# Kernel optimization log

Measured on AMD Instinct MI355X. Metric: run time of the kernel, lower is better.

The kernel has to match this reference:

```python
import jax, jax.numpy as jnp
import numpy as np

B, C, T = 256, 1, 16384   # batch, input_channels, seq_len
H = C                      # hidden_size == input_channels in this module
OUT = 1                    # output_channels


def setup_inputs() -> dict:
    key = jax.random.key(0)
    ks = jax.random.split(key, 11)
    # PyTorch GRU/Linear init: uniform(-1/sqrt(H), 1/sqrt(H)); H=1 -> (-1, 1)
    u = lambda k, shape, s=1.0: jax.random.uniform(k, shape, jnp.float32, -s, s)
    s_lin = 1.0 / np.sqrt(2 * H).astype(np.float32)
    return {
        "x": jax.random.normal(ks[0], (B, C, T), jnp.float32),
        # layer 0: input size C, per direction [3H, C] / [3H, H] / [3H]
        "w_ih0": u(ks[1], (2, 3 * H, C)),
        "w_hh0": u(ks[2], (2, 3 * H, H)),
        "b_ih0": u(ks[3], (2, 3 * H)),
        "b_hh0": u(ks[4], (2, 3 * H)),
        # layers 1-2: input size 2H (bidirectional concat)
        "w_ih12": u(ks[5], (2, 2, 3 * H, 2 * H)),
        "w_hh12": u(ks[6], (2, 2, 3 * H, H)),
        "b_ih12": u(ks[7], (2, 2, 3 * H)),
        "b_hh12": u(ks[8], (2, 2, 3 * H)),
        # output projection Linear(2H -> OUT)
        "w_out": u(ks[9], (OUT, 2 * H), s_lin),
        "b_out": u(ks[10], (OUT,), s_lin),
    }


def _gru_dir(xs, w_ih, w_hh, b_ih, b_hh, reverse):
    """One GRU direction. xs: [T, B, in] -> ys: [T, B, H] (time-aligned)."""
    h0 = jnp.zeros((xs.shape[1], w_hh.shape[1]), xs.dtype)

    def step(h, x_t):
        gi = x_t @ w_ih.T + b_ih          # [B, 3H]
        gh = h @ w_hh.T + b_hh            # [B, 3H]
        ir, iz, inn = jnp.split(gi, 3, axis=-1)
        hr, hz, hn = jnp.split(gh, 3, axis=-1)
        r = jax.nn.sigmoid(ir + hr)
        z = jax.nn.sigmoid(iz + hz)
        n = jnp.tanh(inn + r * hn)
        h_new = (1.0 - z) * n + z * h
        return h_new, h_new

    _, ys = jax.lax.scan(step, h0, xs, reverse=reverse)
    return ys


def _bidir(xs, w_ih_f, w_hh_f, b_ih_f, b_hh_f, w_ih_b, w_hh_b, b_ih_b, b_hh_b):
    fwd = _gru_dir(xs, w_ih_f, w_hh_f, b_ih_f, b_hh_f, reverse=False)
    bwd = _gru_dir(xs, w_ih_b, w_hh_b, b_ih_b, b_hh_b, reverse=True)
    return jnp.concatenate([fwd, bwd], axis=-1)  # [T, B, 2H]


def reference(x, w_ih0, w_hh0, b_ih0, b_hh0, w_ih12, w_hh12, b_ih12, b_hh12, w_out, b_out):
    xs = jnp.transpose(x, (2, 0, 1))  # [B, C, T] -> [T, B, C]
    xs = _bidir(xs, w_ih0[0], w_hh0[0], b_ih0[0], b_hh0[0],
                w_ih0[1], w_hh0[1], b_ih0[1], b_hh0[1])
    for l in range(2):  # GRU layers 1 and 2 (structurally distinct weights)
        xs = _bidir(xs, w_ih12[l, 0], w_hh12[l, 0], b_ih12[l, 0], b_hh12[l, 0],
                    w_ih12[l, 1], w_hh12[l, 1], b_ih12[l, 1], b_hh12[l, 1])
    y = xs @ w_out.T + b_out          # [T, B, OUT]
    return jnp.transpose(y, (1, 2, 0))  # [B, OUT, T]
```

## Files before the change

### kernel.cpp

```cpp
#include <hip/hip_runtime.h>
#include <hip/hip_fp16.h>

#define T_LEN 16384
#define B_SZ  256
#define S_CH  256
#define CL    (T_LEN / S_CH)
#define HALO  32
#define SC    16

__device__ __forceinline__ float ex2(float x)  { return __builtin_amdgcn_exp2f(x); }
__device__ __forceinline__ float rcpf(float x) { return __builtin_amdgcn_rcpf(x); }

__device__ __forceinline__ float gru_step(float h, float preR, float preZ, float preN,
                                          float UR, float UZ, float UN2, float DN2)
{
    float er  = ex2(fmaf(h, UR, preR));
    float ez  = ex2(fmaf(h, UZ, preZ));
    float r   = rcpf(1.0f + er);
    float z   = rcpf(1.0f + ez);
    float hn2 = fmaf(h, UN2, DN2);
    float en  = ex2(fmaf(r, hn2, preN));
    float n   = fmaf(-2.0f, rcpf(1.0f + en), 1.0f);
    float omz = 1.0f - z;
    float zh  = z * h;
    return fmaf(n, omz, zh);
}

template<bool REV>
__device__ __forceinline__ void stageA(const float* __restrict__ x,
        const float* __restrict__ wih, const float* __restrict__ whh,
        const float* __restrict__ bih, const float* __restrict__ bhh,
        __half* __restrict__ l0h, int lane, int b, int a0, int e0)
{
    const int d = REV ? 1 : 0;
    const float L2E = 1.4426950408889634f;
    const float WR  = -L2E * wih[d*3+0];
    const float WZ  = -L2E * wih[d*3+1];
    const float WN  =  2.0f*L2E * wih[d*3+2];
    const float UR  = -L2E * whh[d*3+0];
    const float UZ  = -L2E * whh[d*3+1];
    const float UN2 =  2.0f*L2E * whh[d*3+2];
    const float CR  = -L2E * (bih[d*3+0] + bhh[d*3+0]);
    const float CZ  = -L2E * (bih[d*3+1] + bhh[d*3+1]);
    const float CN  =  2.0f*L2E * bih[d*3+2];
    const float DN2 =  2.0f*L2E * bhh[d*3+2];

    const int warm = REV ? min(HALO, T_LEN - e0) : min(HALO, a0);
    const int nst  = warm + (e0 - a0);
    const int ts   = REV ? (e0 - 1 + warm) : (a0 - warm);
    const float* row = x + (size_t)b * T_LEN;

    float xA[SC], xB[SC];
    float h = 0.0f;

    auto LD = [&](float* F, int base) {
        const float4* p = (const float4*)(row + (REV ? (ts - base - 15) : (ts + base)));
        float4 v0 = p[0], v1 = p[1], v2 = p[2], v3 = p[3];
        float lin[16] = { v0.x,v0.y,v0.z,v0.w, v1.x,v1.y,v1.z,v1.w,
                          v2.x,v2.y,v2.z,v2.w, v3.x,v3.y,v3.z,v3.w };
        #pragma unroll
        for (int k = 0; k < 16; ++k) F[k] = REV ? lin[15 - k] : lin[k];
        __builtin_amdgcn_sched_barrier(0);
    };

    auto CS = [&](float* F, int base) {
        float ov[SC];
        #pragma unroll
        for (int k = 0; k < SC; ++k) {
            float xv = F[k];
            h = gru_step(h, fmaf(xv, WR, CR), fmaf(xv, WZ, CZ), fmaf(xv, WN, CN),
                         UR, UZ, UN2, DN2);
            ov[k] = h;
        }
        if (base >= warm) {
            #pragma unroll
            for (int k = 0; k < SC; ++k) {
                int t = REV ? (ts - (base + k)) : (ts + (base + k));
                l0h[((t - a0) * 64 + lane) * 2 + d] = __float2half_rn(ov[k]);
            }
        }
    };

    LD(xA, 0);
    const int nsup = nst / SC;
    for (int i = 0; i < nsup; i += 2) {
        LD(xB, min((i + 1) * SC, nst - SC));
        CS(xA, i * SC);
        LD(xA, min((i + 2) * SC, nst - SC));
        CS(xB, (i + 1) * SC);
    }
}

template<bool REV>
__device__ __forceinline__ void stageB(const __half* __restrict__ l0h,
        const float* __restrict__ wih, const float* __restrict__ whh,
        const float* __restrict__ bih, const float* __restrict__ bhh,
        __half* __restrict__ l1h, int lane, int a0, int a1, int e1)
{
    const int d = REV ? 1 : 0;
    const float L2E = 1.4426950408889634f;
    const float WR0 = -L2E * wih[(d*3+0)*2+0], WR1 = -L2E * wih[(d*3+0)*2+1];
    const float WZ0 = -L2E * wih[(d*3+1)*2+0], WZ1 = -L2E * wih[(d*3+1)*2+1];
    const float WN0 =  2.0f*L2E * wih[(d*3+2)*2+0], WN1 = 2.0f*L2E * wih[(d*3+2)*2+1];
    const float UR  = -L2E * whh[d*3+0];
    const float UZ  = -L2E * whh[d*3+1];
    const float UN2 =  2.0f*L2E * whh[d*3+2];
    const float CR  = -L2E * (bih[d*3+0] + bhh[d*3+0]);
    const float CZ  = -L2E * (bih[d*3+1] + bhh[d*3+1]);
    const float CN  =  2.0f*L2E * bih[d*3+2];
    const float DN2 =  2.0f*L2E * bhh[d*3+2];

    const int warm = REV ? min(HALO, T_LEN - e1) : min(HALO, a1);
    const int nst  = warm + (e1 - a1);
    const int ts   = REV ? (e1 - 1 + warm) : (a1 - warm);
    const __half2* src = (const __half2*)l0h;

    float fA[SC], gA[SC], fB[SC], gB[SC];
    float h = 0.0f;

#define LDB(F, G, base_) { int base = (base_); \
    _Pragma("unroll") for (int k = 0; k < SC; ++k) { \
      int t = REV ? (ts - (base + k)) : (ts + (base + k)); \
      __half2 v = src[(t - a0) * 64 + lane]; \
      F[k] = __low2float(v); G[k] = __high2float(v); } \
    __builtin_amdgcn_sched_barrier(0); }

#define CSB12(F, G, base_) { int base = (base_); float ov[SC]; \
    _Pragma("unroll") for (int k = 0; k < SC; ++k) { \
      float a = F[k], c = G[k]; \
      float pr = fmaf(a, WR0, fmaf(c, WR1, CR)); \
      float pz = fmaf(a, WZ0, fmaf(c, WZ1, CZ)); \
      float pn = fmaf(a, WN0, fmaf(c, WN1, CN)); \
      h = gru_step(h, pr, pz, pn, UR, UZ, UN2, DN2); ov[k] = h; } \
    if (base >= warm) { \
      _Pragma("unroll") for (int k = 0; k < SC; ++k) { \
        int t = REV ? (ts - (base + k)) : (ts + (base + k)); \
        l1h[((t - a1) * 64 + lane) * 2 + d] = __float2half_rn(ov[k]); } } }

    LDB(fA, gA, 0);
    const int nsup = nst / SC;
    for (int i = 0; i < nsup; i += 2) {
        LDB(fB, gB, min((i + 1) * SC, nst - SC));
        CSB12(fA, gA, i * SC);
        LDB(fA, gA, min((i + 2) * SC, nst - SC));
        CSB12(fB, gB, (i + 1) * SC);
    }
#undef LDB
#undef CSB12
}

__global__ void __launch_bounds__(128) k_all(const float* __restrict__ x,
        const float* __restrict__ w_ih0, const float* __restrict__ w_hh0,
        const float* __restrict__ b_ih0, const float* __restrict__ b_hh0,
        const float* __restrict__ w_ih12, const float* __restrict__ w_hh12,
        const float* __restrict__ b_ih12, const float* __restrict__ b_hh12,
        const float* __restrict__ wo, const float* __restrict__ bo,
        float* __restrict__ y)
{
    __shared__ __align__(16) char smem[81920];
    __half* l0h = (__half*)smem;
    __half* l1h = (__half*)(smem + 49152);
    float (*tY)[65] = (float(*)[65])smem;

    const int blk  = blockIdx.x;
    const int xcd  = blk & 7;
    const int jj   = blk >> 3;
    const int sl   = jj & 31;
    const int bg   = jj >> 5;
    const int s    = xcd * 32 + sl;
    const int lane = threadIdx.x & 63;
    const int w    = threadIdx.x >> 6;
    const int b    = bg * 64 + lane;
    const int sg   = w ? -1 : 1;
    const int t0   = s * CL;

    const int WCf = min(HALO, t0);
    const int WCb = min(HALO, T_LEN - (t0 + CL));
    const int a1  = t0 - WCf, e1 = t0 + CL + WCb;
    const int WBf = min(HALO, a1);
    const int WBb = min(HALO, T_LEN - e1);
    const int a0  = a1 - WBf, e0 = e1 + WBb;

    if (w == 0) stageA<false>(x, w_ih0, w_hh0, b_ih0, b_hh0, l0h, lane, b, a0, e0);
    else        stageA<true >(x, w_ih0, w_hh0, b_ih0, b_hh0, l0h, lane, b, a0, e0);
    __syncthreads();

    if (w == 0) stageB<false>(l0h, w_ih12, w_hh12, b_ih12, b_hh12, l1h, lane, a0, a1, e1);
    else        stageB<true >(l0h, w_ih12, w_hh12, b_ih12, b_hh12, l1h, lane, a0, a1, e1);
    __syncthreads();

    {
        const float* wih = w_ih12 + 12;
        const float* whh = w_hh12 + 6;
        const float* bih = b_ih12 + 6;
        const float* bhh = b_hh12 + 6;
        const int d = w;
        const float L2E = 1.4426950408889634f;
        const float WR0 = -L2E * wih[(d*3+0)*2+0], WR1 = -L2E * wih[(d*3+0)*2+1];
        const float WZ0 = -L2E * wih[(d*3+1)*2+0], WZ1 = -L2E * wih[(d*3+1)*2+1];
        const float WN0 =  2.0f*L2E * wih[(d*3+2)*2+0], WN1 = 2.0f*L2E * wih[(d*3+2)*2+1];
        const float UR  = -L2E * whh[d*3+0];
        const float UZ  = -L2E * whh[d*3+1];
        const float UN2 =  2.0f*L2E * whh[d*3+2];
        const float CR  = -L2E * (bih[d*3+0] + bhh[d*3+0]);
        const float CZ  = -L2E * (bih[d*3+1] + bhh[d*3+1]);
        const float CN  =  2.0f*L2E * bih[d*3+2];
        const float DN2 =  2.0f*L2E * bhh[d*3+2];

        const int warm   = w ? WCb : WCf;
        const int tstart = w ? (e1 - 1) : a1;
        const __half2* src = (const __half2*)l1h;

        float fA[SC], gA[SC], fB[SC], gB[SC];
        float f[CL];
        float h = 0.0f;

#define LD2(F, G, base_) { int base = (base_); \
    _Pragma("unroll") for (int k = 0; k < SC; ++k) { \
      int t = tstart + sg * (base + k); \
      __half2 v = src[(t - a1) * 64 + lane]; \
      F[k] = __low2float(v); G[k] = __high2float(v); } \
    __builtin_amdgcn_sched_barrier(0); }

#define CSB(F, G) { \
    _Pragma("unroll") for (int k = 0; k < SC; ++k) { \
      float a = F[k], c = G[k]; \
      float pr = fmaf(a, WR0, fmaf(c, WR1, CR)); \
      float pz = fmaf(a, WZ0, fmaf(c, WZ1, CZ)); \
      float pn = fmaf(a, WN0, fmaf(c, WN1, CN)); \
      h = gru_step(h, pr, pz, pn, UR, UZ, UN2, DN2); } }

#define CSS(F, G, Q) { \
    _Pragma("unroll") for (int k = 0; k < SC; ++k) { \
      float a = F[k], c = G[k]; \
      float pr = fmaf(a, WR0, fmaf(c, WR1, CR)); \
      float pz = fmaf(a, WZ0, fmaf(c, WZ1, CZ)); \
      float pn = fmaf(a, WN0, fmaf(c, WN1, CN)); \
      h = gru_step(h, pr, pz, pn, UR, UZ, UN2, DN2); \
      f[(Q) * SC + k] = h; } }

        LD2(fA, gA, 0);
        if (warm) {
            LD2(fB, gB, SC);      CSB(fA, gA);
            LD2(fA, gA, 2 * SC);  CSB(fB, gB);
        }
        LD2(fB, gB, warm + SC);      CSS(fA, gA, 0);
        LD2(fA, gA, warm + 2 * SC);  CSS(fB, gB, 1);
        LD2(fB, gB, warm + 3 * SC);  CSS(fA, gA, 2);
                                     CSS(fB, gB, 3);
#undef LD2
#undef CSB
#undef CSS

        const float wf = wo[0], wb = wo[1], bias = bo[0];
        if (w == 0) {
            #pragma unroll
            for (int m = 0; m < CL; ++m) tY[lane][m] = fmaf(wf, f[m], bias);
        }
        __syncthreads();
        if (w == 1) {
            #pragma unroll
            for (int m = 0; m < CL; ++m) tY[lane][CL - 1 - m] += wb * f[m];
        }
        __syncthreads();
        {
            const int b0 = bg * 64;
            const int c4 = threadIdx.x & 15;
            const int r  = (threadIdx.x >> 4) & 7;
            #pragma unroll
            for (int i = 0; i < 8; ++i) {
                int brow = r + 8 * i;
                float4 v = make_float4(tY[brow][c4*4+0], tY[brow][c4*4+1],
                                       tY[brow][c4*4+2], tY[brow][c4*4+3]);
                ((float4*)y)[(size_t)(b0 + brow) * (T_LEN / 4) + (t0 >> 2) + c4] = v;
            }
        }
    }
}

extern "C" void kernel_launch(void* const* d_in, const int* in_sizes, int n_in,
                              void* d_out, int out_size, void* d_ws, size_t ws_size,
                              hipStream_t stream)
{
    (void)in_sizes; (void)n_in; (void)out_size; (void)d_ws; (void)ws_size;
    const float* x      = (const float*)d_in[0];
    const float* w_ih0  = (const float*)d_in[1];
    const float* w_hh0  = (const float*)d_in[2];
    const float* b_ih0  = (const float*)d_in[3];
    const float* b_hh0  = (const float*)d_in[4];
    const float* w_ih12 = (const float*)d_in[5];
    const float* w_hh12 = (const float*)d_in[6];
    const float* b_ih12 = (const float*)d_in[7];
    const float* b_hh12 = (const float*)d_in[8];
    const float* w_out  = (const float*)d_in[9];
    const float* b_out  = (const float*)d_in[10];
    float* y = (float*)d_out;

    k_all<<<4 * S_CH, 128, 0, stream>>>(x, w_ih0, w_hh0, b_ih0, b_hh0,
                                        w_ih12, w_hh12, b_ih12, b_hh12,
                                        w_out, b_out, y);
}
```

Baseline: 144.3 us.

## Fix chunk windows and alias LDS buffers to fit two blocks per CU

Clamps the layer windows to fixed widths (128 for layer 1 output, 192 for layer 0 output) so every block runs the same step count. Layer-1 results are kept in a register buffer and written to shared memory only after a barrier, which lets l1h alias l0h. This cuts LDS from 80KB to about 48KB, and launch_bounds(128,2) asks for two blocks per CU to raise occupancy. In exchange, edge chunks do extra warm-up steps, registers grow by 64 half2 per thread, and the register cap from the second launch bound may cause spills.

```diff
diff --git a/kernel.cpp b/kernel.cpp
--- a/kernel.cpp
+++ b/kernel.cpp
@@ -7,6 +7,8 @@
 #define CL    (T_LEN / S_CH)
 #define HALO  32
 #define SC    16
+#define L1W   128
+#define L0W   192
 
 __device__ __forceinline__ float ex2(float x)  { return __builtin_amdgcn_exp2f(x); }
 __device__ __forceinline__ float rcpf(float x) { return __builtin_amdgcn_rcpf(x); }
@@ -91,65 +93,7 @@
     }
 }
 
-template<bool REV>
-__device__ __forceinline__ void stageB(const __half* __restrict__ l0h,
-        const float* __restrict__ wih, const float* __restrict__ whh,
-        const float* __restrict__ bih, const float* __restrict__ bhh,
-        __half* __restrict__ l1h, int lane, int a0, int a1, int e1)
-{
-    const int d = REV ? 1 : 0;
-    const float L2E = 1.4426950408889634f;
-    const float WR0 = -L2E * wih[(d*3+0)*2+0], WR1 = -L2E * wih[(d*3+0)*2+1];
-    const float WZ0 = -L2E * wih[(d*3+1)*2+0], WZ1 = -L2E * wih[(d*3+1)*2+1];
-    const float WN0 =  2.0f*L2E * wih[(d*3+2)*2+0], WN1 = 2.0f*L2E * wih[(d*3+2)*2+1];
-    const float UR  = -L2E * whh[d*3+0];
-    const float UZ  = -L2E * whh[d*3+1];
-    const float UN2 =  2.0f*L2E * whh[d*3+2];
-    const float CR  = -L2E * (bih[d*3+0] + bhh[d*3+0]);
-    const float CZ  = -L2E * (bih[d*3+1] + bhh[d*3+1]);
-    const float CN  =  2.0f*L2E * bih[d*3+2];
-    const float DN2 =  2.0f*L2E * bhh[d*3+2];
-
-    const int warm = REV ? min(HALO, T_LEN - e1) : min(HALO, a1);
-    const int nst  = warm + (e1 - a1);
-    const int ts   = REV ? (e1 - 1 + warm) : (a1 - warm);
-    const __half2* src = (const __half2*)l0h;
-
-    float fA[SC], gA[SC], fB[SC], gB[SC];
-    float h = 0.0f;
-
-#define LDB(F, G, base_) { int base = (base_); \
-    _Pragma("unroll") for (int k = 0; k < SC; ++k) { \
-      int t = REV ? (ts - (base + k)) : (ts + (base + k)); \
-      __half2 v = src[(t - a0) * 64 + lane]; \
-      F[k] = __low2float(v); G[k] = __high2float(v); } \
-    __builtin_amdgcn_sched_barrier(0); }
-
-#define CSB12(F, G, base_) { int base = (base_); float ov[SC]; \
-    _Pragma("unroll") for (int k = 0; k < SC; ++k) { \
-      float a = F[k], c = G[k]; \
-      float pr = fmaf(a, WR0, fmaf(c, WR1, CR)); \
-      float pz = fmaf(a, WZ0, fmaf(c, WZ1, CZ)); \
-      float pn = fmaf(a, WN0, fmaf(c, WN1, CN)); \
-      h = gru_step(h, pr, pz, pn, UR, UZ, UN2, DN2); ov[k] = h; } \
-    if (base >= warm) { \
-      _Pragma("unroll") for (int k = 0; k < SC; ++k) { \
-        int t = REV ? (ts - (base + k)) : (ts + (base + k)); \
-        l1h[((t - a1) * 64 + lane) * 2 + d] = __float2half_rn(ov[k]); } } }
-
-    LDB(fA, gA, 0);
-    const int nsup = nst / SC;
-    for (int i = 0; i < nsup; i += 2) {
-        LDB(fB, gB, min((i + 1) * SC, nst - SC));
-        CSB12(fA, gA, i * SC);
-        LDB(fA, gA, min((i + 2) * SC, nst - SC));
-        CSB12(fB, gB, (i + 1) * SC);
-    }
-#undef LDB
-#undef CSB12
-}
-
-__global__ void __launch_bounds__(128) k_all(const float* __restrict__ x,
+__global__ void __launch_bounds__(128, 2) k_all(const float* __restrict__ x,
         const float* __restrict__ w_ih0, const float* __restrict__ w_hh0,
         const float* __restrict__ b_ih0, const float* __restrict__ b_hh0,
         const float* __restrict__ w_ih12, const float* __restrict__ w_hh12,
@@ -157,10 +101,10 @@
         const float* __restrict__ wo, const float* __restrict__ bo,
         float* __restrict__ y)
 {
-    __shared__ __align__(16) char smem[81920];
+    __shared__ __align__(16) char smem[49408];
     __half* l0h = (__half*)smem;
-    __half* l1h = (__half*)(smem + 49152);
-    float (*tY)[65] = (float(*)[65])smem;
+    __half* l1h = (__half*)smem;
+    float (*tY)[65] = (float(*)[65])(smem + 32768);
 
     const int blk  = blockIdx.x;
     const int xcd  = blk & 7;
@@ -174,20 +118,101 @@
     const int sg   = w ? -1 : 1;
     const int t0   = s * CL;
 
-    const int WCf = min(HALO, t0);
-    const int WCb = min(HALO, T_LEN - (t0 + CL));
-    const int a1  = t0 - WCf, e1 = t0 + CL + WCb;
-    const int WBf = min(HALO, a1);
-    const int WBb = min(HALO, T_LEN - e1);
-    const int a0  = a1 - WBf, e0 = e1 + WBb;
+    int a1 = t0 - HALO;
+    a1 = a1 < 0 ? 0 : (a1 > T_LEN - L1W ? T_LEN - L1W : a1);
+    const int e1 = a1 + L1W;
+    int a0 = a1 - HALO;
+    a0 = a0 < 0 ? 0 : (a0 > T_LEN - L0W ? T_LEN - L0W : a0);
+    const int e0 = a0 + L0W;
+
+    const float L2E = 1.4426950408889634f;
 
     if (w == 0) stageA<false>(x, w_ih0, w_hh0, b_ih0, b_hh0, l0h, lane, b, a0, e0);
     else        stageA<true >(x, w_ih0, w_hh0, b_ih0, b_hh0, l0h, lane, b, a0, e0);
     __syncthreads();
 
-    if (w == 0) stageB<false>(l0h, w_ih12, w_hh12, b_ih12, b_hh12, l1h, lane, a0, a1, e1);
-    else        stageB<true >(l0h, w_ih12, w_hh12, b_ih12, b_hh12, l1h, lane, a0, a1, e1);
-    __syncthreads();
+    {
+        const int d = w;
+        const float WR0 = -L2E * w_ih12[(d*3+0)*2+0], WR1 = -L2E * w_ih12[(d*3+0)*2+1];
+        const float WZ0 = -L2E * w_ih12[(d*3+1)*2+0], WZ1 = -L2E * w_ih12[(d*3+1)*2+1];
+        const float WN0 =  2.0f*L2E * w_ih12[(d*3+2)*2+0], WN1 = 2.0f*L2E * w_ih12[(d*3+2)*2+1];
+        const float UR  = -L2E * w_hh12[d*3+0];
+        const float UZ  = -L2E * w_hh12[d*3+1];
+        const float UN2 =  2.0f*L2E * w_hh12[d*3+2];
+        const float CR  = -L2E * (b_ih12[d*3+0] + b_hh12[d*3+0]);
+        const float CZ  = -L2E * (b_ih12[d*3+1] + b_hh12[d*3+1]);
+        const float CN  =  2.0f*L2E * b_ih12[d*3+2];
+        const float DN2 =  2.0f*L2E * b_hh12[d*3+2];
+
+        const int warmB = w ? (e0 - e1) : (a1 - a0);
+        const int tsB   = w ? (e0 - 1) : a0;
+        const __half2* src = (const __half2*)l0h;
+
+        float fA[SC], gA[SC], fB[SC], gB[SC];
+        __half2 l1buf[64];
+        float h = 0.0f;
+
+#define LDB(F, G, base_) { int base = (base_); \
+    _Pragma("unroll") for (int k = 0; k < SC; ++k) { \
+      int t = tsB + sg * (base + k); \
+      __half2 v = src[(t - a0) * 64 + lane]; \
+      F[k] = __low2float(v); G[k] = __high2float(v); } \
+    __builtin_amdgcn_sched_barrier(0); }
+
+#define CSN(F, G) { \
+    _Pragma("unroll") for (int k = 0; k < SC; ++k) { \
+      float a = F[k], c = G[k]; \
+      float pr = fmaf(a, WR0, fmaf(c, WR1, CR)); \
+      float pz = fmaf(a, WZ0, fmaf(c, WZ1, CZ)); \
+      float pn = fmaf(a, WN0, fmaf(c, WN1, CN)); \
+      h = gru_step(h, pr, pz, pn, UR, UZ, UN2, DN2); } }
+
+#define CST(F, G, Q) { float ov[SC]; \
+    _Pragma("unroll") for (int k = 0; k < SC; ++k) { \
+      float a = F[k], c = G[k]; \
+      float pr = fmaf(a, WR0, fmaf(c, WR1, CR)); \
+      float pz = fmaf(a, WZ0, fmaf(c, WZ1, CZ)); \
+      float pn = fmaf(a, WN0, fmaf(c, WN1, CN)); \
+      h = gru_step(h, pr, pz, pn, UR, UZ, UN2, DN2); ov[k] = h; } \
+    _Pragma("unroll") for (int k2 = 0; k2 < SC/2; ++k2) \
+      l1buf[(Q)*8 + k2] = __halves2half2(__float2half_rn(ov[2*k2]), \
+                                         __float2half_rn(ov[2*k2+1])); }
+
+        LDB(fA, gA, 0);
+        for (int i = 0; i < warmB / SC; i += 2) {
+            LDB(fB, gB, (i + 1) * SC);  CSN(fA, gA);
+            LDB(fA, gA, (i + 2) * SC);  CSN(fB, gB);
+        }
+        LDB(fB, gB, warmB + 1*SC);  CST(fA, gA, 0);
+        LDB(fA, gA, warmB + 2*SC);  CST(fB, gB, 1);
+        LDB(fB, gB, warmB + 3*SC);  CST(fA, gA, 2);
+        LDB(fA, gA, warmB + 4*SC);  CST(fB, gB, 3);
+        LDB(fB, gB, warmB + 5*SC);  CST(fA, gA, 4);
+        LDB(fA, gA, warmB + 6*SC);  CST(fB, gB, 5);
+        LDB(fB, gB, warmB + 7*SC);  CST(fA, gA, 6);
+                                    CST(fB, gB, 7);
+#undef LDB
+#undef CSN
+#undef CST
+
+        __syncthreads();
+        if (w == 0) {
+            #pragma unroll
+            for (int j = 0; j < 64; ++j) {
+                __half2 v = l1buf[j];
+                l1h[((2*j    ) * 64 + lane) * 2 + 0] = __low2half(v);
+                l1h[((2*j + 1) * 64 + lane) * 2 + 0] = __high2half(v);
+            }
+        } else {
+            #pragma unroll
+            for (int j = 0; j < 64; ++j) {
+                __half2 v = l1buf[j];
+                l1h[((127 - 2*j) * 64 + lane) * 2 + 1] = __low2half(v);
+                l1h[((126 - 2*j) * 64 + lane) * 2 + 1] = __high2half(v);
+            }
+        }
+        __syncthreads();
+    }
 
     {
         const float* wih = w_ih12 + 12;
@@ -195,7 +220,6 @@
         const float* bih = b_ih12 + 6;
         const float* bhh = b_hh12 + 6;
         const int d = w;
-        const float L2E = 1.4426950408889634f;
         const float WR0 = -L2E * wih[(d*3+0)*2+0], WR1 = -L2E * wih[(d*3+0)*2+1];
         const float WZ0 = -L2E * wih[(d*3+1)*2+0], WZ1 = -L2E * wih[(d*3+1)*2+1];
         const float WN0 =  2.0f*L2E * wih[(d*3+2)*2+0], WN1 = 2.0f*L2E * wih[(d*3+2)*2+1];
@@ -207,7 +231,7 @@
         const float CN  =  2.0f*L2E * bih[d*3+2];
         const float DN2 =  2.0f*L2E * bhh[d*3+2];
 
-        const int warm   = w ? WCb : WCf;
+        const int warmC  = w ? (e1 - (t0 + CL)) : (t0 - a1);
         const int tstart = w ? (e1 - 1) : a1;
         const __half2* src = (const __half2*)l1h;
 
@@ -240,14 +264,14 @@
       f[(Q) * SC + k] = h; } }
 
         LD2(fA, gA, 0);
-        if (warm) {
-            LD2(fB, gB, SC);      CSB(fA, gA);
-            LD2(fA, gA, 2 * SC);  CSB(fB, gB);
-        }
-        LD2(fB, gB, warm + SC);      CSS(fA, gA, 0);
-        LD2(fA, gA, warm + 2 * SC);  CSS(fB, gB, 1);
-        LD2(fB, gB, warm + 3 * SC);  CSS(fA, gA, 2);
-                                     CSS(fB, gB, 3);
+        for (int i = 0; i < warmC / SC; i += 2) {
+            LD2(fB, gB, (i + 1) * SC);  CSB(fA, gA);
+            LD2(fA, gA, (i + 2) * SC);  CSB(fB, gB);
+        }
+        LD2(fB, gB, warmC + 1*SC);  CSS(fA, gA, 0);
+        LD2(fA, gA, warmC + 2*SC);  CSS(fB, gB, 1);
+        LD2(fB, gB, warmC + 3*SC);  CSS(fA, gA, 2);
+                                    CSS(fB, gB, 3);
 #undef LD2
 #undef CSB
 #undef CSS
```

Measured after the change: 166.5 us. +15.4%, slower.
